# Kernel tuning notes

Hardware: AMD Instinct MI355X
Metric: run time of the kernel (lower is better)

The kernel has to match this reference:

```python
import jax, jax.numpy as jnp
import numpy as np

ITE = 20
LAM = 0.1
MU1 = 0.1
MU2 = 0.1
RHO = 1.05
SHAPE = (4, 31, 128, 128)  # N, C, H, W


def setup_inputs() -> dict:
    key = jax.random.key(0)
    k1, k2 = jax.random.split(key)
    Y = jax.random.normal(k1, SHAPE, dtype=jnp.float32)
    inW = jax.random.uniform(k2, SHAPE, dtype=jnp.float32)  # positive weights (W^2)
    return {"Y": Y, "inW": inW}


def _shrink(x, t):
    # soft-threshold: sign(x) * max(|x| - t, 0)
    return jnp.sign(x) * jnp.maximum(jnp.abs(x) - t, 0.0)


def _diff_h(x):
    # circular convolution with kernel [1, -1] along width
    return x - jnp.roll(x, 1, axis=-1)


def _diff_v(x):
    # circular convolution with kernel [[1], [-1]] along height
    return x - jnp.roll(x, 1, axis=-2)


def reference(Y, inW):
    H, W = Y.shape[-2], Y.shape[-1]
    # p2o: PSF placed at top-left of (H, W) canvas, then fft2
    dh = jnp.zeros((H, W), jnp.float32).at[0, 0].set(1.0).at[0, 1].set(-1.0)
    dv = jnp.zeros((H, W), jnp.float32).at[0, 0].set(1.0).at[1, 0].set(-1.0)
    FH = jnp.fft.fft2(dh)
    FV = jnp.fft.fft2(dv)
    demo = jnp.abs(FH) ** 2 + jnp.abs(FV) ** 2  # [H, W] real
    FHc = jnp.conj(FH)
    FVc = jnp.conj(FV)

    def tv_solver(A, B, C, mu1, mu2):
        # Fourier-domain solve of (mu1 I + mu2 D^T D) Z = mu1 A + mu2 D^T [B; C]
        num = mu1 * jnp.fft.fft2(A) + mu2 * (FHc * jnp.fft.fft2(B) + FVc * jnp.fft.fft2(C))
        return jnp.real(jnp.fft.ifft2(num / (mu1 + mu2 * demo)))

    zeros = jnp.zeros_like(Y)
    carry = (Y, Y, zeros, zeros, zeros, _diff_h(Y), _diff_v(Y),
             jnp.float32(MU1), jnp.float32(MU2))

    def body(c, _):
        Z, X, G1, G21, G22, DhZ, DvZ, mu1, mu2 = c
        Uh = _shrink(DhZ - G21 / mu2, LAM / mu2)
        Uv = _shrink(DvZ - G22 / mu2, LAM / mu2)
        Z = tv_solver(X + G1 / mu1, Uh + G21 / mu2, Uv + G22 / mu2, mu1, mu2)
        DhZ = _diff_h(Z)
        DvZ = _diff_v(Z)
        X = (inW * Y + mu1 * Z - G1) / (inW + mu1)
        G1 = G1 + mu1 * (X - Z)
        G21 = G21 + mu2 * (Uh - DhZ)
        G22 = G22 + mu2 * (Uv - DvZ)
        return (Z, X, G1, G21, G22, DhZ, DvZ, RHO * mu1, RHO * mu2), None

    (Z, *_), _ = jax.lax.scan(body, carry, None, length=ITE)
    return Z
```

## Files before the change

kernel.cpp:

```cpp
#include <hip/hip_runtime.h>


#define NPIX   16384
#define NSIDE  128
#define NIMG   124
#define NT     1024
#define PXT    16
#define N_ITE  20
#define LAM_F  0.1f
#define RHO_F  1.05f
#define PI_F   3.14159265358979323846f

#define SW(c) ((c) ^ ((c) >> 3))

__device__ __forceinline__ float2 cadd(float2 a, float2 b) {
    return make_float2(a.x + b.x, a.y + b.y);
}
__device__ __forceinline__ float2 csub(float2 a, float2 b) {
    return make_float2(a.x - b.x, a.y - b.y);
}
__device__ __forceinline__ float2 cmul(float2 a, float2 w) {
    return make_float2(fmaf(a.x, w.x, -(a.y * w.y)),
                       fmaf(a.x, w.y,  (a.y * w.x)));
}
__device__ __forceinline__ float2 cmulc(float2 a, float2 w) {
    return make_float2(fmaf(a.x, w.x,  (a.y * w.y)),
                       fmaf(a.y, w.x, -(a.x * w.y)));
}

__global__ __launch_bounds__(NT, 4) void hwtv_kernel(
    const float* __restrict__ Yg,
    const float* __restrict__ Wg,
    float* __restrict__ outg)
{
    extern __shared__ char smem[];
    float2* C  = (float2*)smem;
    float2* TW = (float2*)(smem + (size_t)NPIX * 8);
    float*  D1 = (float*)(smem + (size_t)NPIX * 8 + 64*8);

    const int tid = threadIdx.x;
    const size_t base  = (size_t)blockIdx.x * NPIX;
    const float* Y  = Yg + base;
    const float* Wt = Wg + base;
    float* out = outg + base;

    if (tid < 64) {
        float ang = -2.0f * PI_F * (float)tid / 128.0f;
        TW[tid] = make_float2(cosf(ang), sinf(ang));
    }
    if (tid < 128) {
        int br = (int)(__brev((unsigned)tid) >> 25);
        float s = sinf(PI_F * (float)br / 128.0f);
        D1[tid] = 4.0f * s * s;
    }

    float a[PXT], g1[PXT], bh[PXT], bv[PXT];
    #pragma unroll
    for (int k = 0; k < PXT; ++k) {
        int p = tid + k * NT;
        int col = p & (NSIDE - 1);
        int rowb = p & ~(NSIDE - 1);
        float y = Y[p];
        C[rowb + SW(col)] = make_float2(y, 0.0f);
        a[k]  = 0.1f * y;
        g1[k] = 0.0f;
        bh[k] = 0.0f;
        bv[k] = 0.0f;
    }
    __syncthreads();

    float mu1 = 0.1f, mu2 = 0.1f;

    for (int it = 0; it < N_ITE; ++it) {
        const float mu2p   = mu2 * (1.0f / RHO_F);
        const float inv_m2 = 1.0f / mu2;
        const float thr    = LAM_F * inv_m2;

        #pragma unroll 4
        for (int k = 0; k < PXT; ++k) {
            int p    = tid + k * NT;
            int col  = p & (NSIDE - 1);
            int rowb = p & ~(NSIDE - 1);
            int sc_  = SW(col);
            float z  = C[rowb + sc_].x;
            float zl = C[rowb + SW((col + NSIDE - 1) & (NSIDE - 1))].x;
            int pu   = (p + NPIX - NSIDE) & (NPIX - 1);
            float zu = C[(pu & ~(NSIDE - 1)) + sc_].x;
            float dhz = z - zl;
            float dvz = z - zu;
            float g21 = (it == 0) ? 0.0f : fmaf(-mu2p, dhz, bh[k]);
            float g22 = (it == 0) ? 0.0f : fmaf(-mu2p, dvz, bv[k]);
            float ah = dhz - g21 * inv_m2;
            float av = dvz - g22 * inv_m2;
            float uh = copysignf(fmaxf(fabsf(ah) - thr, 0.0f), ah);
            float uv = copysignf(fmaxf(fabsf(av) - thr, 0.0f), av);
            bh[k] = fmaf(mu2, uh, g21);
            bv[k] = fmaf(mu2, uv, g22);
        }
        __syncthreads();

        #pragma unroll 4
        for (int k = 0; k < PXT; ++k) {
            int p = tid + k * NT;
            int col = p & (NSIDE - 1);
            int rowb = p & ~(NSIDE - 1);
            C[rowb + SW(col)] = make_float2(bh[k], bv[k]);
        }
        __syncthreads();

        float numv[PXT];
        #pragma unroll 4
        for (int k = 0; k < PXT; ++k) {
            int p    = tid + k * NT;
            int col  = p & (NSIDE - 1);
            int rowb = p & ~(NSIDE - 1);
            int sc_  = SW(col);
            float bhr = C[rowb + SW((col + 1) & (NSIDE - 1))].x;
            int pd    = (p + NSIDE) & (NPIX - 1);
            float bvd = C[(pd & ~(NSIDE - 1)) + sc_].y;
            numv[k] = a[k] + (bh[k] - bhr) + (bv[k] - bvd);
        }
        __syncthreads();

        #pragma unroll 4
        for (int k = 0; k < PXT; ++k) {
            int p = tid + k * NT;
            int col = p & (NSIDE - 1);
            int rowb = p & ~(NSIDE - 1);
            C[rowb + SW(col)] = make_float2(numv[k], 0.0f);
        }
        __syncthreads();

        #define FWD_ROW_PASS(S, L2)                                          \
        {                                                                    \
            _Pragma("unroll 2")                                              \
            for (int q = 0; q < 4; ++q) {                                    \
                int m   = tid + q * NT;                                      \
                int rb  = (m >> 5) << 7;                                     \
                int b   = m & 31;                                            \
                int j   = b & ((L2) - 1);                                    \
                int i0  = ((b & ~((L2) - 1)) << 2) | j;                      \
                int e0 = rb + SW(i0);                                        \
                int e1 = rb + SW(i0 + (L2));                                 \
                int e2 = rb + SW(i0 + 2*(L2));                               \
                int e3 = rb + SW(i0 + 3*(L2));                               \
                float2 w1 = TW[j << (S)];                                    \
                float2 w2 = cmul(w1, w1);                                    \
                float2 x0 = C[e0], x1 = C[e1];                               \
                float2 x2 = C[e2], x3 = C[e3];                               \
                float2 t02p = cadd(x0, x2);                                  \
                float2 t13p = cadd(x1, x3);                                  \
                float2 t02m = cmul(csub(x0, x2), w1);                        \
                float2 uu   = cmul(csub(x1, x3), w1);                        \
                float2 t13m = make_float2(uu.y, -uu.x);          \
                C[e0] = cadd(t02p, t13p);                                    \
                C[e1] = cmul(csub(t02p, t13p), w2);                          \
                C[e2] = cadd(t02m, t13m);                                    \
                C[e3] = cmul(csub(t02m, t13m), w2);                          \
            }                                                                \
            __syncthreads();                                                 \
        }
        FWD_ROW_PASS(0, 32)
        FWD_ROW_PASS(2, 8)
        FWD_ROW_PASS(4, 2)
        #pragma unroll 4
        for (int q = 0; q < 8; ++q) {
            int tau = tid + q * NT;
            int t   = tau & 63;
            int org = (tau >> 6) << 7;
            int c0  = t << 1;
            int ea  = org + SW(c0);
            int eb  = org + SW(c0 + 1);
            float2 A = C[ea], B = C[eb];
            C[ea] = cadd(A, B);
            C[eb] = csub(A, B);
        }
        __syncthreads();

        #define FWD_COL_PASS(S, L2)                                          \
        {                                                                    \
            _Pragma("unroll 2")                                              \
            for (int q = 0; q < 4; ++q) {                                    \
                int m  = tid + q * NT;                                       \
                int c  = m & 127;                                            \
                int b  = m >> 7;                                             \
                int j  = b & ((L2) - 1);                                     \
                int i0 = ((b & ~((L2) - 1)) << 2) | j;                       \
                int p0 = (i0 << 7) + SW(c);                                  \
                const int ST = (L2) << 7;                                    \
                float2 w1 = TW[j << (S)];                                    \
                float2 w2 = cmul(w1, w1);                                    \
                float2 x0 = C[p0], x1 = C[p0 + ST];                          \
                float2 x2 = C[p0 + 2*ST], x3 = C[p0 + 3*ST];                 \
                float2 t02p = cadd(x0, x2);                                  \
                float2 t13p = cadd(x1, x3);                                  \
                float2 t02m = cmul(csub(x0, x2), w1);                        \
                float2 uu   = cmul(csub(x1, x3), w1);                        \
                float2 t13m = make_float2(uu.y, -uu.x);                      \
                C[p0]        = cadd(t02p, t13p);                             \
                C[p0 +   ST] = cmul(csub(t02p, t13p), w2);                   \
                C[p0 + 2*ST] = cadd(t02m, t13m);                             \
                C[p0 + 3*ST] = cmul(csub(t02m, t13m), w2);                   \
            }                                                                \
            __syncthreads();                                                 \
        }
        FWD_COL_PASS(0, 32)
        FWD_COL_PASS(2, 8)
        FWD_COL_PASS(4, 2)

        {
            const float sc = 1.0f / (float)NPIX;
            #pragma unroll 4
            for (int q = 0; q < 8; ++q) {
                int tau = tid + q * NT;
                int c   = tau & 127;
                int t   = tau >> 7;
                int r0  = t << 1;
                int p0  = (r0 << 7) + SW(c);
                float2 A = C[p0], B = C[p0 + NSIDE];
                float2 s2 = cadd(A, B);
                float2 d2 = csub(A, B);
                float d1c = D1[c];
                float f0 = sc / fmaf(mu2, D1[r0]     + d1c, mu1);
                float f1 = sc / fmaf(mu2, D1[r0 + 1] + d1c, mu1);
                s2.x *= f0; s2.y *= f0;
                d2.x *= f1; d2.y *= f1;
                C[p0]         = cadd(s2, d2);
                C[p0 + NSIDE] = csub(s2, d2);
            }
            __syncthreads();
        }

        #define INV_COL_PASS(SB, M)                                          \
        {                                                                    \
            _Pragma("unroll 2")                                              \
            for (int q = 0; q < 4; ++q) {                                    \
                int m  = tid + q * NT;                                       \
                int c  = m & 127;                                            \
                int b  = m >> 7;                                             \
                int j  = b & ((M) - 1);                                      \
                int i0 = ((b & ~((M) - 1)) << 2) | j;                        \
                int p0 = (i0 << 7) + SW(c);                                  \
                const int ST = (M) << 7;                                     \
                float2 wb = TW[j << (SB)];                                   \
                float2 wa = cmul(wb, wb);                                    \
                float2 x0 = C[p0], x1 = C[p0 + ST];                          \
                float2 x2 = C[p0 + 2*ST], x3 = C[p0 + 3*ST];                 \
                float2 pp1 = cmulc(x1, wa);                                  \
                float2 a0 = cadd(x0, pp1), a1 = csub(x0, pp1);               \
                float2 pp2 = cmulc(x3, wa);                                  \
                float2 a2 = cadd(x2, pp2), a3 = csub(x2, pp2);               \
                float2 q0 = cmulc(a2, wb);                                   \
                float2 y0 = cadd(a0, q0), y2 = csub(a0, q0);                 \
                float2 uu = cmulc(a3, wb);                                   \
                float2 q1 = make_float2(-uu.y, uu.x);            \
                float2 y1 = cadd(a1, q1), y3 = csub(a1, q1);                 \
                C[p0]        = y0;                                           \
                C[p0 +   ST] = y1;                                           \
                C[p0 + 2*ST] = y2;                                           \
                C[p0 + 3*ST] = y3;                                           \
            }                                                                \
            __syncthreads();                                                 \
        }
        INV_COL_PASS(4, 2)
        INV_COL_PASS(2, 8)
        INV_COL_PASS(0, 32)

        #pragma unroll 4
        for (int q = 0; q < 8; ++q) {
            int tau = tid + q * NT;
            int t   = tau & 63;
            int org = (tau >> 6) << 7;
            int c0  = t << 1;
            int ea  = org + SW(c0);
            int eb  = org + SW(c0 + 1);
            float2 A = C[ea], B = C[eb];
            C[ea] = cadd(A, B);
            C[eb] = csub(A, B);
        }
        __syncthreads();
        #define INV_ROW_PASS(SB, M)                                          \
        {                                                                    \
            _Pragma("unroll 2")                                              \
            for (int q = 0; q < 4; ++q) {                                    \
                int m   = tid + q * NT;                                      \
                int rb  = (m >> 5) << 7;                                     \
                int b   = m & 31;                                            \
                int j   = b & ((M) - 1);                                     \
                int i0  = ((b & ~((M) - 1)) << 2) | j;                       \
                int e0 = rb + SW(i0);                                        \
                int e1 = rb + SW(i0 + (M));                                  \
                int e2 = rb + SW(i0 + 2*(M));                                \
                int e3 = rb + SW(i0 + 3*(M));                                \
                float2 wb = TW[j << (SB)];                                   \
                float2 wa = cmul(wb, wb);                                    \
                float2 x0 = C[e0], x1 = C[e1];                               \
                float2 x2 = C[e2], x3 = C[e3];                               \
                float2 pp1 = cmulc(x1, wa);                                  \
                float2 a0 = cadd(x0, pp1), a1 = csub(x0, pp1);               \
                float2 pp2 = cmulc(x3, wa);                                  \
                float2 a2 = cadd(x2, pp2), a3 = csub(x2, pp2);               \
                float2 q0 = cmulc(a2, wb);                                   \
                float2 y0 = cadd(a0, q0), y2 = csub(a0, q0);                 \
                float2 uu = cmulc(a3, wb);                                   \
                float2 q1 = make_float2(-uu.y, uu.x);                        \
                float2 y1 = cadd(a1, q1), y3 = csub(a1, q1);                 \
                C[e0] = y0;                                                  \
                C[e1] = y1;                                                  \
                C[e2] = y2;                                                  \
                C[e3] = y3;                                                  \
            }                                                                \
            __syncthreads();                                                 \
        }
        INV_ROW_PASS(4, 2)
        INV_ROW_PASS(2, 8)
        INV_ROW_PASS(0, 32)

        const float mu1n = mu1 * RHO_F;
        #pragma unroll 4
        for (int k = 0; k < PXT; ++k) {
            int p = tid + k * NT;
            int col = p & (NSIDE - 1);
            int rowb = p & ~(NSIDE - 1);
            float z  = C[rowb + SW(col)].x;
            float y  = Y[p];
            float w  = Wt[p];
            float x  = fmaf(w, y, fmaf(mu1, z, -g1[k])) *
                       __builtin_amdgcn_rcpf(w + mu1);
            g1[k] = fmaf(mu1, x - z, g1[k]);
            a[k]  = fmaf(mu1n, x, g1[k]);
            if (it == N_ITE - 1) out[p] = z;
        }

        mu1 *= RHO_F;
        mu2 *= RHO_F;
    }
}

extern "C" void kernel_launch(void* const* d_in, const int* in_sizes, int n_in,
                              void* d_out, int out_size, void* d_ws, size_t ws_size,
                              hipStream_t stream) {
    (void)in_sizes; (void)n_in; (void)out_size; (void)d_ws; (void)ws_size;
    const float* Y   = (const float*)d_in[0];
    const float* inW = (const float*)d_in[1];
    float* out = (float*)d_out;

    const size_t smem_bytes = (size_t)NPIX * 8 + 64 * 8 + 128 * 4;
    hipFuncSetAttribute((const void*)hwtv_kernel,
                        hipFuncAttributeMaxDynamicSharedMemorySize,
                        (int)smem_bytes);
    hipLaunchKernelGGL(hwtv_kernel, dim3(NIMG), dim3(NT), smem_bytes, stream,
                       Y, inW, out);
}
```

Baseline: 779.0 us.

## Merge final radix-4 and radix-2 FFT stages into register radix-8 passes

Replaces the last radix-4 pass plus the radix-2 pass in the row and column FFTs, forward and inverse, with a single radix-8 butterfly held in registers. The spectral divide is folded between the column forward and inverse radix-8 steps. This removes several shared-memory round trips and __syncthreads barriers per iteration. In exchange each thread holds more registers (8 complex values) and reads strided or swizzled addresses that may cause bank conflicts.

```diff
diff --git a/kernel.cpp b/kernel.cpp
--- a/kernel.cpp
+++ b/kernel.cpp
@@ -26,6 +26,52 @@
 __device__ __forceinline__ float2 cmulc(float2 a, float2 w) {
     return make_float2(fmaf(a.x, w.x,  (a.y * w.y)),
                        fmaf(a.y, w.x, -(a.x * w.y)));
+}
+
+#define RT2H 0.70710678118654752f
+
+__device__ __forceinline__ void radix8_fwd(float2 z[8]) {
+    float2 A0 = cadd(z[0], z[4]), A1 = cadd(z[1], z[5]);
+    float2 A2 = cadd(z[2], z[6]), A3 = cadd(z[3], z[7]);
+    float2 d0 = csub(z[0], z[4]), d1 = csub(z[1], z[5]);
+    float2 d2 = csub(z[2], z[6]), d3 = csub(z[3], z[7]);
+    float2 B0 = d0;
+    float2 B1 = make_float2(RT2H*(d1.x + d1.y), RT2H*(d1.y - d1.x));
+    float2 B2 = make_float2(d2.y, -d2.x);
+    float2 B3 = make_float2(RT2H*(d3.y - d3.x), -RT2H*(d3.x + d3.y));
+    float2 C0 = cadd(A0, A2), C2 = csub(A0, A2);
+    float2 t13 = csub(A1, A3);
+    float2 C1 = cadd(A1, A3);
+    float2 C3 = make_float2(t13.y, -t13.x);
+    float2 E0 = cadd(B0, B2), E2 = csub(B0, B2);
+    float2 u13 = csub(B1, B3);
+    float2 E1 = cadd(B1, B3);
+    float2 E3 = make_float2(u13.y, -u13.x);
+    z[0] = cadd(C0, C1);  z[1] = csub(C0, C1);
+    z[2] = cadd(C2, C3);  z[3] = csub(C2, C3);
+    z[4] = cadd(E0, E1);  z[5] = csub(E0, E1);
+    z[6] = cadd(E2, E3);  z[7] = csub(E2, E3);
+}
+
+__device__ __forceinline__ void radix8_inv(float2 z[8]) {
+    float2 a0 = cadd(z[0], z[1]), a1 = csub(z[0], z[1]);
+    float2 a2 = cadd(z[2], z[3]), a3 = csub(z[2], z[3]);
+    float2 a4 = cadd(z[4], z[5]), a5 = csub(z[4], z[5]);
+    float2 a6 = cadd(z[6], z[7]), a7 = csub(z[6], z[7]);
+    float2 b0 = cadd(a0, a2), b2 = csub(a0, a2);
+    float2 t3 = make_float2(-a3.y, a3.x);
+    float2 b1 = cadd(a1, t3), b3 = csub(a1, t3);
+    float2 b4 = cadd(a4, a6), b6 = csub(a4, a6);
+    float2 t7 = make_float2(-a7.y, a7.x);
+    float2 b5 = cadd(a5, t7), b7 = csub(a5, t7);
+    float2 p0 = b4;
+    float2 p1 = make_float2(RT2H*(b5.x - b5.y), RT2H*(b5.x + b5.y));
+    float2 p2 = make_float2(-b6.y, b6.x);
+    float2 p3 = make_float2(-RT2H*(b7.x + b7.y), RT2H*(b7.x - b7.y));
+    z[0] = cadd(b0, p0);  z[4] = csub(b0, p0);
+    z[1] = cadd(b1, p1);  z[5] = csub(b1, p1);
+    z[2] = cadd(b2, p2);  z[6] = csub(b2, p2);
+    z[3] = cadd(b3, p3);  z[7] = csub(b3, p3);
 }
 
 __global__ __launch_bounds__(NT, 4) void hwtv_kernel(
@@ -162,20 +208,21 @@
         }
         FWD_ROW_PASS(0, 32)
         FWD_ROW_PASS(2, 8)
-        FWD_ROW_PASS(4, 2)
-        #pragma unroll 4
-        for (int q = 0; q < 8; ++q) {
-            int tau = tid + q * NT;
-            int t   = tau & 63;
-            int org = (tau >> 6) << 7;
-            int c0  = t << 1;
-            int ea  = org + SW(c0);
-            int eb  = org + SW(c0 + 1);
-            float2 A = C[ea], B = C[eb];
-            C[ea] = cadd(A, B);
-            C[eb] = csub(A, B);
-        }
-        __syncthreads();
+        {
+            #pragma unroll 2
+            for (int q = 0; q < 2; ++q) {
+                int m  = tid + q * NT;
+                int rb = (m >> 4) << 7;
+                int cb = (m & 15) << 3;
+                float2 z[8];
+                #pragma unroll
+                for (int i = 0; i < 8; ++i) z[i] = C[rb + SW(cb + i)];
+                radix8_fwd(z);
+                #pragma unroll
+                for (int i = 0; i < 8; ++i) C[rb + SW(cb + i)] = z[i];
+            }
+            __syncthreads();
+        }
 
         #define FWD_COL_PASS(S, L2)                                          \
         {                                                                    \
@@ -206,27 +253,29 @@
         }
         FWD_COL_PASS(0, 32)
         FWD_COL_PASS(2, 8)
-        FWD_COL_PASS(4, 2)
 
         {
             const float sc = 1.0f / (float)NPIX;
-            #pragma unroll 4
-            for (int q = 0; q < 8; ++q) {
-                int tau = tid + q * NT;
-                int c   = tau & 127;
-                int t   = tau >> 7;
-                int r0  = t << 1;
-                int p0  = (r0 << 7) + SW(c);
-                float2 A = C[p0], B = C[p0 + NSIDE];
-                float2 s2 = cadd(A, B);
-                float2 d2 = csub(A, B);
-                float d1c = D1[c];
-                float f0 = sc / fmaf(mu2, D1[r0]     + d1c, mu1);
-                float f1 = sc / fmaf(mu2, D1[r0 + 1] + d1c, mu1);
-                s2.x *= f0; s2.y *= f0;
-                d2.x *= f1; d2.y *= f1;
-                C[p0]         = cadd(s2, d2);
-                C[p0 + NSIDE] = csub(s2, d2);
+            #pragma unroll 2
+            for (int q = 0; q < 2; ++q) {
+                int m   = tid + q * NT;
+                int col = m & 127;
+                int g   = m >> 7;
+                int r0  = g << 3;
+                int p0  = (r0 << 7) + SW(col);
+                float2 z[8];
+                #pragma unroll
+                for (int i = 0; i < 8; ++i) z[i] = C[p0 + (i << 7)];
+                radix8_fwd(z);
+                float d1c = D1[col];
+                #pragma unroll
+                for (int i = 0; i < 8; ++i) {
+                    float f = sc / fmaf(mu2, D1[r0 + i] + d1c, mu1);
+                    z[i].x *= f; z[i].y *= f;
+                }
+                radix8_inv(z);
+                #pragma unroll
+                for (int i = 0; i < 8; ++i) C[p0 + (i << 7)] = z[i];
             }
             __syncthreads();
         }
@@ -262,23 +311,24 @@
             }                                                                \
             __syncthreads();                                                 \
         }
-        INV_COL_PASS(4, 2)
         INV_COL_PASS(2, 8)
         INV_COL_PASS(0, 32)
 
-        #pragma unroll 4
-        for (int q = 0; q < 8; ++q) {
-            int tau = tid + q * NT;
-            int t   = tau & 63;
-            int org = (tau >> 6) << 7;
-            int c0  = t << 1;
-            int ea  = org + SW(c0);
-            int eb  = org + SW(c0 + 1);
-            float2 A = C[ea], B = C[eb];
-            C[ea] = cadd(A, B);
-            C[eb] = csub(A, B);
-        }
-        __syncthreads();
+        {
+            #pragma unroll 2
+            for (int q = 0; q < 2; ++q) {
+                int m  = tid + q * NT;
+                int rb = (m >> 4) << 7;
+                int cb = (m & 15) << 3;
+                float2 z[8];
+                #pragma unroll
+                for (int i = 0; i < 8; ++i) z[i] = C[rb + SW(cb + i)];
+                radix8_inv(z);
+                #pragma unroll
+                for (int i = 0; i < 8; ++i) C[rb + SW(cb + i)] = z[i];
+            }
+            __syncthreads();
+        }
         #define INV_ROW_PASS(SB, M)                                          \
         {                                                                    \
             _Pragma("unroll 2")                                              \
@@ -312,7 +362,6 @@
             }                                                                \
             __syncthreads();                                                 \
         }
-        INV_ROW_PASS(4, 2)
         INV_ROW_PASS(2, 8)
         INV_ROW_PASS(0, 32)
 
```

After: 660.8 us. 1.18x faster.
